# Performance work log

Hardware: AMD Instinct MI355X
Metric: run time of the kernel (lower is better)

## Reference

```python
import jax, jax.numpy as jnp
import numpy as np

A_BITS = 8
W_BITS = 8
STRIDE = 1
PADDING = 1


def _quant_dequant(t, bits):
    """Symmetric per-tensor min-max quantize-dequantize to `bits` bits.

    This is the math the PCILT lookup-table conv realizes: every LUT entry is
    (quantized activation level) * (quantized weight level), so summing LUT
    entries over the conv window == conv(x_qdq, w_qdq).
    """
    qmax = 2.0 ** (bits - 1) - 1.0
    scale = jnp.maximum(jnp.max(jnp.abs(t)) / qmax, 1e-8)
    return jnp.clip(jnp.round(t / scale), -qmax, qmax) * scale


def setup_inputs() -> dict:
    key = jax.random.key(0)
    k1, k2 = jax.random.split(key)
    x = jax.random.normal(k1, (16, 64, 112, 112), dtype=jnp.float32)  # NCHW
    W = jax.random.normal(k2, (128, 64, 3, 3), dtype=jnp.float32) * 0.05  # OIHW
    return {"x": x, "W": W}


def reference(x, W):
    xq = _quant_dequant(x, A_BITS)
    wq = _quant_dequant(W, W_BITS)
    out = jax.lax.conv_general_dilated(
        xq, wq,
        window_strides=(STRIDE, STRIDE),
        padding=[(PADDING, PADDING), (PADDING, PADDING)],
        dimension_numbers=("NCHW", "OIHW", "NCHW"))
    return out  # [16, 128, 112, 112]
```

## Files before the change

### kernel.cpp

```cpp
#include <hip/hip_runtime.h>
#include <hip/hip_bf16.h>


typedef __attribute__((ext_vector_type(8))) short short8;
typedef __attribute__((ext_vector_type(4))) int   int4v;
typedef __attribute__((ext_vector_type(4))) float f32x4;
typedef __attribute__((ext_vector_type(4))) float float4v;
typedef __attribute__((ext_vector_type(8)))  signed char char8;
typedef __attribute__((ext_vector_type(16))) signed char char16;

#define N_IMG 16
#define C_IN 64
#define HW 112
#define O_CH 128
#define WPITCH 576
#define XPITCH 80
#define TP 72
#define NPART 3136

__global__ __launch_bounds__(256) void absmax_part(const float* __restrict__ x,
                                                   const float* __restrict__ w,
                                                   float* __restrict__ part) {
    const int b = blockIdx.x, tid = threadIdx.x;
    const float4v* x4 = (const float4v*)x;
    const long base = (long)b * 1024 + tid;
    const float4v v0 = x4[base];
    const float4v v1 = x4[base + 256];
    const float4v v2 = x4[base + 512];
    const float4v v3 = x4[base + 768];
    float mx = fmaxf(fmaxf(fmaxf(fabsf(v0.x), fabsf(v0.y)), fmaxf(fabsf(v0.z), fabsf(v0.w))),
                     fmaxf(fmaxf(fabsf(v1.x), fabsf(v1.y)), fmaxf(fabsf(v1.z), fabsf(v1.w))));
    mx = fmaxf(mx, fmaxf(fmaxf(fabsf(v2.x), fabsf(v2.y)), fmaxf(fabsf(v2.z), fabsf(v2.w))));
    mx = fmaxf(mx, fmaxf(fmaxf(fabsf(v3.x), fabsf(v3.y)), fmaxf(fabsf(v3.z), fabsf(v3.w))));
    float mw = 0.f;
    if (b < 72) {
        const float4v q = ((const float4v*)w)[b * 256 + tid];
        mw = fmaxf(fmaxf(fabsf(q.x), fabsf(q.y)), fmaxf(fabsf(q.z), fabsf(q.w)));
    }
    #pragma unroll
    for (int off = 32; off > 0; off >>= 1) {
        mx = fmaxf(mx, __shfl_down(mx, off));
        mw = fmaxf(mw, __shfl_down(mw, off));
    }
    __shared__ float smx[4], smw[4];
    const int wave = tid >> 6, lane = tid & 63;
    if (lane == 0) { smx[wave] = mx; smw[wave] = mw; }
    __syncthreads();
    if (tid == 0) {
        part[b]         = fmaxf(fmaxf(smx[0], smx[1]), fmaxf(smx[2], smx[3]));
        part[NPART + b] = fmaxf(fmaxf(smw[0], smw[1]), fmaxf(smw[2], smw[3]));
    }
}

__global__ __launch_bounds__(256) void reduce_scal(const float* __restrict__ part,
                                                   unsigned* __restrict__ scal) {
    const int tid = threadIdx.x;
    float mx = 0.f, mw = 0.f;
    for (int i = tid; i < NPART; i += 256) {
        mx = fmaxf(mx, part[i]);
        mw = fmaxf(mw, part[NPART + i]);
    }
    #pragma unroll
    for (int off = 32; off > 0; off >>= 1) {
        mx = fmaxf(mx, __shfl_down(mx, off));
        mw = fmaxf(mw, __shfl_down(mw, off));
    }
    __shared__ float smx[4], smw[4];
    const int wave = tid >> 6, lane = tid & 63;
    if (lane == 0) { smx[wave] = mx; smw[wave] = mw; }
    __syncthreads();
    if (tid == 0) {
        scal[0] = __float_as_uint(fmaxf(fmaxf(smx[0], smx[1]), fmaxf(smx[2], smx[3])));
        scal[1] = __float_as_uint(fmaxf(fmaxf(smw[0], smw[1]), fmaxf(smw[2], smw[3])));
    }
}

__global__ __launch_bounds__(256) void quant_w(const float* __restrict__ w,
                                               const unsigned* __restrict__ scal,
                                               signed char* __restrict__ wt8) {
    const int idx = blockIdx.x * 256 + threadIdx.x;
    if (idx >= O_CH * C_IN * 9) return;
    const float sw = fmaxf(__uint_as_float(scal[1]) * (1.f / 127.f), 1e-8f);
    const int kw = idx % 3;
    int t = idx / 3;
    const int kh = t % 3;
    t /= 3;
    const int c = t % C_IN;
    const int o = t / C_IN;
    float v = rintf(w[idx] / sw);
    v = fminf(fmaxf(v, -127.f), 127.f);
    wt8[o * WPITCH + (kh * 3 + kw) * C_IN + c] = (signed char)(int)v;
}

__global__ __launch_bounds__(256) void quant_x(const float* __restrict__ x,
                                               const unsigned* __restrict__ scal,
                                               signed char* __restrict__ xq8) {
    __shared__ __align__(16) short tile[HW * TP];
    const int tid = threadIdx.x;
    const int n = blockIdx.x / HW, h = blockIdx.x % HW;
    const float inv_sx = 1.f / fmaxf(__uint_as_float(scal[0]) * (1.f / 127.f), 1e-8f);
    #pragma unroll
    for (int i = 0; i < 7; ++i) {
        const int l = i * 256 + tid;
        const int c = l / 28, w4 = l - c * 28;
        const float4v v = *(const float4v*)(x + ((long)(n * C_IN + c) * HW + h) * HW + w4 * 4);
        float q[4];
        q[0] = fminf(fmaxf(rintf(v.x * inv_sx), -127.f), 127.f);
        q[1] = fminf(fmaxf(rintf(v.y * inv_sx), -127.f), 127.f);
        q[2] = fminf(fmaxf(rintf(v.z * inv_sx), -127.f), 127.f);
        q[3] = fminf(fmaxf(rintf(v.w * inv_sx), -127.f), 127.f);
        const int osw = ((c >> 3) ^ (w4 & 7)) * 8 + (c & 7);
        #pragma unroll
        for (int j = 0; j < 4; ++j)
            tile[(w4 * 4 + j) * TP + osw] = (short)q[j];
    }
    __syncthreads();
    const int g = tid & 3, wi = tid >> 2;
    signed char* dst = xq8 + (long)(n * HW + h) * HW * C_IN;
    #pragma unroll
    for (int j = 0; j < 2; ++j) {
        const int w = j * 64 + wi;
        if (w < HW) {
            const int sw = (w >> 2) & 7;
            const short8 s0 = *(const short8*)(tile + w * TP + ((2 * g) ^ sw) * 8);
            const short8 s1 = *(const short8*)(tile + w * TP + ((2 * g + 1) ^ sw) * 8);
            const char8 c0 = __builtin_convertvector(s0, char8);
            const char8 c1 = __builtin_convertvector(s1, char8);
            const char16 cc = __builtin_shufflevector(c0, c1,
                0, 1, 2, 3, 4, 5, 6, 7, 8, 9, 10, 11, 12, 13, 14, 15);
            *(char16*)(dst + w * C_IN + g * 16) = cc;
        }
    }
}

__global__ __launch_bounds__(256, 4) void conv_kernel(const signed char* __restrict__ xq8,
                                                      const signed char* __restrict__ wt8,
                                                      const unsigned* __restrict__ scal,
                                                      float* __restrict__ out) {
    __shared__ __align__(16) signed char xs[3 * 114 * XPITCH];
    const int tid = threadIdx.x;
    const int wave = tid >> 6, lane = tid & 63;
    const int quad = lane >> 4, l16 = lane & 15;
    const int lin = (blockIdx.x & 7) * 224 + (blockIdx.x >> 3);
    const int n = lin / HW, oh = lin % HW;

    if (tid < 24) {
        const int r = tid >> 3, col = (tid >> 2) & 1, c16 = tid & 3;
        *(int4v*)(xs + (r * 114 + col * 113) * XPITCH + c16 * 16) = (int4v)0;
    }
    #pragma unroll
    for (int it = 0; it < 6; ++it) {
        const int gph = it * 256 + tid;
        if (gph < 1344) {
            const int r = gph / 448, rem = gph - r * 448;
            const int ow = rem >> 2, c16 = rem & 3;
            const int ih = oh - 1 + r;
            int4v v = (int4v)0;
            if ((unsigned)ih < (unsigned)HW)
                v = *(const int4v*)(xq8 + ((long)(n * HW + ih) * HW + ow) * C_IN + c16 * 16);
            *(int4v*)(xs + (r * 114 + ow + 1) * XPITCH + c16 * 16) = v;
        }
    }

    int4v acc[7][2];
    #pragma unroll
    for (int mt = 0; mt < 7; ++mt) { acc[mt][0] = (int4v)0; acc[mt][1] = (int4v)0; }

    const signed char* wrow0 = wt8 + (wave * 32 + l16) * WPITCH + quad * 16;
    const signed char* wrow1 = wrow0 + 16 * WPITCH;

    int4v bcur0 = *(const int4v*)(wrow0);
    int4v bcur1 = *(const int4v*)(wrow1);
    int4v bnxt0, bnxt1;

    __syncthreads();

    #pragma unroll
    for (int tap = 0; tap < 9; ++tap) {
        if (tap < 8) {
            bnxt0 = *(const int4v*)(wrow0 + (tap + 1) * C_IN);
            bnxt1 = *(const int4v*)(wrow1 + (tap + 1) * C_IN);
        }
        const signed char* rowb = xs + ((tap / 3) * 114 + (tap % 3) + l16) * XPITCH + quad * 16;
        #pragma unroll
        for (int mt = 0; mt < 7; ++mt) {
            const int4v afr = *(const int4v*)(rowb + mt * (16 * XPITCH));
            acc[mt][0] = __builtin_amdgcn_mfma_i32_16x16x64_i8(afr, bcur0, acc[mt][0], 0, 0, 0);
            acc[mt][1] = __builtin_amdgcn_mfma_i32_16x16x64_i8(afr, bcur1, acc[mt][1], 0, 0, 0);
        }
        bcur0 = bnxt0;
        bcur1 = bnxt1;
    }

    const float s = fmaxf(__uint_as_float(scal[0]) * (1.f / 127.f), 1e-8f) *
                    fmaxf(__uint_as_float(scal[1]) * (1.f / 127.f), 1e-8f);
    #pragma unroll
    for (int mt = 0; mt < 7; ++mt) {
        #pragma unroll
        for (int ot = 0; ot < 2; ++ot) {
            const int o = wave * 32 + ot * 16 + l16;
            const int mrow = mt * 16 + quad * 4;
            const f32x4 v = __builtin_convertvector(acc[mt][ot], f32x4) * s;
            *(f32x4*)(out + (((long)(n * O_CH + o) * HW + oh) * HW + mrow)) = v;
        }
    }
}

extern "C" void kernel_launch(void* const* d_in, const int* in_sizes, int n_in,
                              void* d_out, int out_size, void* d_ws, size_t ws_size,
                              hipStream_t stream) {
    const float* x = (const float*)d_in[0];
    const float* W = (const float*)d_in[1];
    float* out = (float*)d_out;

    unsigned* scal = (unsigned*)d_ws;
    signed char* wt8 = (signed char*)((char*)d_ws + 1024);
    signed char* xq8 = (signed char*)((char*)d_ws + 76800);
    float* part = (float*)xq8;

    hipLaunchKernelGGL(absmax_part, dim3(NPART), dim3(256), 0, stream, x, W, part);
    hipLaunchKernelGGL(reduce_scal, dim3(1), dim3(256), 0, stream, part, scal);
    hipLaunchKernelGGL(quant_w, dim3(288), dim3(256), 0, stream, W, scal, wt8);
    hipLaunchKernelGGL(quant_x, dim3(N_IMG * HW), dim3(256), 0, stream, x, scal, xq8);
    hipLaunchKernelGGL(conv_kernel, dim3(N_IMG * HW), dim3(256), 0, stream, xq8, wt8, scal, out);
}
```

Measured before the change: 171.9 us.

## Fuse scale reduction and quantization kernels; compute two output rows per conv block

Merges the single-block reduce_scal, quant_w and quant_x into one kernel. Every block redundantly reduces the partial maxima itself, and only the first 72 weight partials are read, since weight partials are only nonzero there. The partial maxima now live in the output buffer, so they no longer overlap the quantized activations that the fused kernel writes. The conv kernel stages four input rows and computes two output rows per block, halving the grid and reusing the shared halo rows. This trades two launches and some redundant row loads for redundant per-block partial reads and more LDS per block.

```diff
diff --git a/kernel.cpp b/kernel.cpp
--- a/kernel.cpp
+++ b/kernel.cpp
@@ -52,53 +52,55 @@
     }
 }
 
-__global__ __launch_bounds__(256) void reduce_scal(const float* __restrict__ part,
-                                                   unsigned* __restrict__ scal) {
+__global__ __launch_bounds__(256) void quant_wx(const float* __restrict__ x,
+                                                const float* __restrict__ w,
+                                                const float* __restrict__ part,
+                                                unsigned* __restrict__ scal,
+                                                signed char* __restrict__ wt8,
+                                                signed char* __restrict__ xq8) {
+    __shared__ __align__(16) short tile[HW * TP];
+    __shared__ float smx[4], smw[4];
     const int tid = threadIdx.x;
+    const int wave = tid >> 6, lane = tid & 63;
+
     float mx = 0.f, mw = 0.f;
-    for (int i = tid; i < NPART; i += 256) {
-        mx = fmaxf(mx, part[i]);
-        mw = fmaxf(mw, part[NPART + i]);
-    }
+    #pragma unroll
+    for (int i = 0; i < 13; ++i) {
+        const int idx = i * 256 + tid;
+        if (idx < NPART) mx = fmaxf(mx, part[idx]);
+    }
+    if (tid < 72) mw = part[NPART + tid];
     #pragma unroll
     for (int off = 32; off > 0; off >>= 1) {
         mx = fmaxf(mx, __shfl_down(mx, off));
         mw = fmaxf(mw, __shfl_down(mw, off));
     }
-    __shared__ float smx[4], smw[4];
-    const int wave = tid >> 6, lane = tid & 63;
     if (lane == 0) { smx[wave] = mx; smw[wave] = mw; }
     __syncthreads();
-    if (tid == 0) {
-        scal[0] = __float_as_uint(fmaxf(fmaxf(smx[0], smx[1]), fmaxf(smx[2], smx[3])));
-        scal[1] = __float_as_uint(fmaxf(fmaxf(smw[0], smw[1]), fmaxf(smw[2], smw[3])));
-    }
-}
-
-__global__ __launch_bounds__(256) void quant_w(const float* __restrict__ w,
-                                               const unsigned* __restrict__ scal,
-                                               signed char* __restrict__ wt8) {
-    const int idx = blockIdx.x * 256 + threadIdx.x;
-    if (idx >= O_CH * C_IN * 9) return;
-    const float sw = fmaxf(__uint_as_float(scal[1]) * (1.f / 127.f), 1e-8f);
-    const int kw = idx % 3;
-    int t = idx / 3;
-    const int kh = t % 3;
-    t /= 3;
-    const int c = t % C_IN;
-    const int o = t / C_IN;
-    float v = rintf(w[idx] / sw);
-    v = fminf(fmaxf(v, -127.f), 127.f);
-    wt8[o * WPITCH + (kh * 3 + kw) * C_IN + c] = (signed char)(int)v;
-}
-
-__global__ __launch_bounds__(256) void quant_x(const float* __restrict__ x,
-                                               const unsigned* __restrict__ scal,
-                                               signed char* __restrict__ xq8) {
-    __shared__ __align__(16) short tile[HW * TP];
-    const int tid = threadIdx.x;
+    const float xm = fmaxf(fmaxf(smx[0], smx[1]), fmaxf(smx[2], smx[3]));
+    const float wm = fmaxf(fmaxf(smw[0], smw[1]), fmaxf(smw[2], smw[3]));
+    const float sx = fmaxf(xm * (1.f / 127.f), 1e-8f);
+    const float sw = fmaxf(wm * (1.f / 127.f), 1e-8f);
+    if (blockIdx.x == 0 && tid == 0) {
+        scal[0] = __float_as_uint(xm);
+        scal[1] = __float_as_uint(wm);
+    }
+
+    if (blockIdx.x < 288) {
+        const int idx = blockIdx.x * 256 + tid;
+        const int kw = idx % 3;
+        int t = idx / 3;
+        const int kh = t % 3;
+        t /= 3;
+        const int c = t % C_IN;
+        const int o = t / C_IN;
+        float v = rintf(w[idx] / sw);
+        v = fminf(fmaxf(v, -127.f), 127.f);
+        wt8[o * WPITCH + (kh * 3 + kw) * C_IN + c] = (signed char)(int)v;
+    }
+
     const int n = blockIdx.x / HW, h = blockIdx.x % HW;
-    const float inv_sx = 1.f / fmaxf(__uint_as_float(scal[0]) * (1.f / 127.f), 1e-8f);
+    const float inv_sx = 1.f / sx;
     #pragma unroll
     for (int i = 0; i < 7; ++i) {
         const int l = i * 256 + tid;
@@ -119,16 +121,16 @@
     signed char* dst = xq8 + (long)(n * HW + h) * HW * C_IN;
     #pragma unroll
     for (int j = 0; j < 2; ++j) {
-        const int w = j * 64 + wi;
-        if (w < HW) {
-            const int sw = (w >> 2) & 7;
-            const short8 s0 = *(const short8*)(tile + w * TP + ((2 * g) ^ sw) * 8);
-            const short8 s1 = *(const short8*)(tile + w * TP + ((2 * g + 1) ^ sw) * 8);
+        const int ww = j * 64 + wi;
+        if (ww < HW) {
+            const int sw2 = (ww >> 2) & 7;
+            const short8 s0 = *(const short8*)(tile + ww * TP + ((2 * g) ^ sw2) * 8);
+            const short8 s1 = *(const short8*)(tile + ww * TP + ((2 * g + 1) ^ sw2) * 8);
             const char8 c0 = __builtin_convertvector(s0, char8);
             const char8 c1 = __builtin_convertvector(s1, char8);
             const char16 cc = __builtin_shufflevector(c0, c1,
                 0, 1, 2, 3, 4, 5, 6, 7, 8, 9, 10, 11, 12, 13, 14, 15);
-            *(char16*)(dst + w * C_IN + g * 16) = cc;
+            *(char16*)(dst + ww * C_IN + g * 16) = cc;
         }
     }
 }
@@ -137,71 +139,73 @@
                                                       const signed char* __restrict__ wt8,
                                                       const unsigned* __restrict__ scal,
                                                       float* __restrict__ out) {
-    __shared__ __align__(16) signed char xs[3 * 114 * XPITCH];
+    __shared__ __align__(16) signed char xs[4 * 114 * XPITCH];
     const int tid = threadIdx.x;
     const int wave = tid >> 6, lane = tid & 63;
     const int quad = lane >> 4, l16 = lane & 15;
-    const int lin = (blockIdx.x & 7) * 224 + (blockIdx.x >> 3);
-    const int n = lin / HW, oh = lin % HW;
-
-    if (tid < 24) {
+    const int lin = (blockIdx.x & 7) * 112 + (blockIdx.x >> 3);
+    const int n = lin / 56, oh0 = (lin % 56) * 2;
+
+    if (tid < 32) {
         const int r = tid >> 3, col = (tid >> 2) & 1, c16 = tid & 3;
         *(int4v*)(xs + (r * 114 + col * 113) * XPITCH + c16 * 16) = (int4v)0;
     }
     #pragma unroll
-    for (int it = 0; it < 6; ++it) {
+    for (int it = 0; it < 7; ++it) {
         const int gph = it * 256 + tid;
-        if (gph < 1344) {
-            const int r = gph / 448, rem = gph - r * 448;
-            const int ow = rem >> 2, c16 = rem & 3;
-            const int ih = oh - 1 + r;
-            int4v v = (int4v)0;
-            if ((unsigned)ih < (unsigned)HW)
-                v = *(const int4v*)(xq8 + ((long)(n * HW + ih) * HW + ow) * C_IN + c16 * 16);
-            *(int4v*)(xs + (r * 114 + ow + 1) * XPITCH + c16 * 16) = v;
-        }
-    }
-
-    int4v acc[7][2];
-    #pragma unroll
-    for (int mt = 0; mt < 7; ++mt) { acc[mt][0] = (int4v)0; acc[mt][1] = (int4v)0; }
+        const int r = gph / 448, rem = gph - r * 448;
+        const int ow = rem >> 2, c16 = rem & 3;
+        const int ih = oh0 - 1 + r;
+        int4v v = (int4v)0;
+        if ((unsigned)ih < (unsigned)HW)
+            v = *(const int4v*)(xq8 + ((long)(n * HW + ih) * HW + ow) * C_IN + c16 * 16);
+        *(int4v*)(xs + (r * 114 + ow + 1) * XPITCH + c16 * 16) = v;
+    }
 
     const signed char* wrow0 = wt8 + (wave * 32 + l16) * WPITCH + quad * 16;
     const signed char* wrow1 = wrow0 + 16 * WPITCH;
-
-    int4v bcur0 = *(const int4v*)(wrow0);
-    int4v bcur1 = *(const int4v*)(wrow1);
-    int4v bnxt0, bnxt1;
-
-    __syncthreads();
-
-    #pragma unroll
-    for (int tap = 0; tap < 9; ++tap) {
-        if (tap < 8) {
-            bnxt0 = *(const int4v*)(wrow0 + (tap + 1) * C_IN);
-            bnxt1 = *(const int4v*)(wrow1 + (tap + 1) * C_IN);
-        }
-        const signed char* rowb = xs + ((tap / 3) * 114 + (tap % 3) + l16) * XPITCH + quad * 16;
-        #pragma unroll
-        for (int mt = 0; mt < 7; ++mt) {
-            const int4v afr = *(const int4v*)(rowb + mt * (16 * XPITCH));
-            acc[mt][0] = __builtin_amdgcn_mfma_i32_16x16x64_i8(afr, bcur0, acc[mt][0], 0, 0, 0);
-            acc[mt][1] = __builtin_amdgcn_mfma_i32_16x16x64_i8(afr, bcur1, acc[mt][1], 0, 0, 0);
-        }
-        bcur0 = bnxt0;
-        bcur1 = bnxt1;
-    }
-
     const float s = fmaxf(__uint_as_float(scal[0]) * (1.f / 127.f), 1e-8f) *
                     fmaxf(__uint_as_float(scal[1]) * (1.f / 127.f), 1e-8f);
-    #pragma unroll
-    for (int mt = 0; mt < 7; ++mt) {
-        #pragma unroll
-        for (int ot = 0; ot < 2; ++ot) {
-            const int o = wave * 32 + ot * 16 + l16;
-            const int mrow = mt * 16 + quad * 4;
-            const f32x4 v = __builtin_convertvector(acc[mt][ot], f32x4) * s;
-            *(f32x4*)(out + (((long)(n * O_CH + o) * HW + oh) * HW + mrow)) = v;
+
+    __syncthreads();
+
+    #pragma unroll
+    for (int p = 0; p < 2; ++p) {
+        int4v acc[7][2];
+        #pragma unroll
+        for (int mt = 0; mt < 7; ++mt) { acc[mt][0] = (int4v)0; acc[mt][1] = (int4v)0; }
+
+        int4v bcur0 = *(const int4v*)(wrow0);
+        int4v bcur1 = *(const int4v*)(wrow1);
+        int4v bnxt0, bnxt1;
+
+        #pragma unroll
+        for (int tap = 0; tap < 9; ++tap) {
+            if (tap < 8) {
+                bnxt0 = *(const int4v*)(wrow0 + (tap + 1) * C_IN);
+                bnxt1 = *(const int4v*)(wrow1 + (tap + 1) * C_IN);
+            }
+            const signed char* rowb = xs + ((p + tap / 3) * 114 + (tap % 3) + l16) * XPITCH + quad * 16;
+            #pragma unroll
+            for (int mt = 0; mt < 7; ++mt) {
+                const int4v afr = *(const int4v*)(rowb + mt * (16 * XPITCH));
+                acc[mt][0] = __builtin_amdgcn_mfma_i32_16x16x64_i8(afr, bcur0, acc[mt][0], 0, 0, 0);
+                acc[mt][1] = __builtin_amdgcn_mfma_i32_16x16x64_i8(afr, bcur1, acc[mt][1], 0, 0, 0);
+            }
+            bcur0 = bnxt0;
+            bcur1 = bnxt1;
+        }
+
+        const int oh = oh0 + p;
+        #pragma unroll
+        for (int mt = 0; mt < 7; ++mt) {
+            #pragma unroll
+            for (int ot = 0; ot < 2; ++ot) {
+                const int o = wave * 32 + ot * 16 + l16;
+                const int mrow = mt * 16 + quad * 4;
+                const f32x4 v = __builtin_convertvector(acc[mt][ot], f32x4) * s;
+                *(f32x4*)(out + (((long)(n * O_CH + o) * HW + oh) * HW + mrow)) = v;
+            }
         }
     }
 }
@@ -216,11 +220,10 @@
     unsigned* scal = (unsigned*)d_ws;
     signed char* wt8 = (signed char*)((char*)d_ws + 1024);
     signed char* xq8 = (signed char*)((char*)d_ws + 76800);
-    float* part = (float*)xq8;
+    float* part = (float*)out;
 
     hipLaunchKernelGGL(absmax_part, dim3(NPART), dim3(256), 0, stream, x, W, part);
-    hipLaunchKernelGGL(reduce_scal, dim3(1), dim3(256), 0, stream, part, scal);
-    hipLaunchKernelGGL(quant_w, dim3(288), dim3(256), 0, stream, W, scal, wt8);
-    hipLaunchKernelGGL(quant_x, dim3(N_IMG * HW), dim3(256), 0, stream, x, scal, xq8);
-    hipLaunchKernelGGL(conv_kernel, dim3(N_IMG * HW), dim3(256), 0, stream, xq8, wt8, scal, out);
-}
+    hipLaunchKernelGGL(quant_wx, dim3(N_IMG * HW), dim3(256), 0, stream,
+                       x, W, part, scal, wt8, xq8);
+    hipLaunchKernelGGL(conv_kernel, dim3(896), dim3(256), 0, stream, xq8, wt8, scal, out);
+}
```

Result: no change. 168.8 us (-1.8%).
